# Kernel tuning notes

Hardware: AMD Instinct MI355X
Metric: run time of the kernel (lower is better)

## Reference

```python
import jax, jax.numpy as jnp
import numpy as np

NUM_TOKENS = 2048
HIDDEN = 2048
MOE_INTER = 1408
N_EXPERTS = 16
TOP_K = 4
N_SHARED = 2
SHARED_INTER = N_SHARED * MOE_INTER  # 2816
CAPACITY = 768
ROUTED_SCALE = 1.0


def setup_inputs() -> dict:
    key = jax.random.key(0)
    ks = jax.random.split(key, 9)
    s = 0.02  # init scale for stability
    return {
        "hidden_states": jax.random.normal(ks[0], (NUM_TOKENS, HIDDEN), jnp.float32),
        "w_gate": jax.random.normal(ks[1], (N_EXPERTS, HIDDEN), jnp.float32) * s,
        "w1": jax.random.normal(ks[2], (N_EXPERTS, HIDDEN, MOE_INTER), jnp.float32) * s,  # gate_proj
        "w3": jax.random.normal(ks[3], (N_EXPERTS, HIDDEN, MOE_INTER), jnp.float32) * s,  # up_proj
        "w2": jax.random.normal(ks[4], (N_EXPERTS, MOE_INTER, HIDDEN), jnp.float32) * s,  # down_proj
        "ws1": jax.random.normal(ks[5], (HIDDEN, SHARED_INTER), jnp.float32) * s,
        "ws3": jax.random.normal(ks[6], (HIDDEN, SHARED_INTER), jnp.float32) * s,
        "ws2": jax.random.normal(ks[7], (SHARED_INTER, HIDDEN), jnp.float32) * s,
    }


def _moe_forward(x, w_gate, w1, w3, w2, ws1, ws3, ws2):
    T, d = x.shape
    E = w1.shape[0]
    # ---- router: softmax scores, top-k selection (DeepSeek-V2, norm_topk_prob=False) ----
    scores = jax.nn.softmax(x @ w_gate.T, axis=-1)            # [T, E]
    topw, topi = jax.lax.top_k(scores, TOP_K)                 # [T, K]
    topw = topw * ROUTED_SCALE
    flat_e = topi.reshape(-1)                                 # [T*K] expert id per slot
    flat_w = topw.reshape(-1)                                 # [T*K]
    tok_ids = jnp.repeat(jnp.arange(T), TOP_K)                # [T*K]
    # ---- dispatch: position of each slot within its expert's buffer ----
    onehot = jax.nn.one_hot(flat_e, E, dtype=jnp.int32)       # [T*K, E]
    pos = jnp.take_along_axis(jnp.cumsum(onehot, axis=0), flat_e[:, None], axis=1)[:, 0] - 1
    valid = (pos < CAPACITY).astype(x.dtype)
    buf = jnp.zeros((E, CAPACITY, d), x.dtype).at[flat_e, pos].set(x[tok_ids], mode='drop')
    # ---- grouped SwiGLU expert FFN ----
    g = jnp.einsum('ecd,edi->eci', buf, w1)
    u = jnp.einsum('ecd,edi->eci', buf, w3)
    o = jnp.einsum('eci,eid->ecd', jax.nn.silu(g) * u, w2)    # [E, C, d]
    # ---- combine: gather back, weight, scatter-add per token ----
    gathered = o[flat_e, jnp.clip(pos, 0, CAPACITY - 1)] * (flat_w * valid)[:, None]
    routed = jax.ops.segment_sum(gathered, tok_ids, num_segments=T)  # [T, d]
    # ---- shared experts (always-on SwiGLU) ----
    shared = (jax.nn.silu(x @ ws1) * (x @ ws3)) @ ws2
    return routed + shared


def reference(hidden_states, w_gate, w1, w3, w2, ws1, ws3, ws2):
    return _moe_forward(hidden_states, w_gate, w1, w3, w2, ws1, ws3, ws2)
```

## Files before the change

kernel.cpp:

```cpp
#include <hip/hip_runtime.h>
#include <hip/hip_bf16.h>
#include <cstdint>

#define T_TOKENS 2048
#define HIDDEN 2048
#define INTER 1408
#define NEXP 16
#define TOPK 4
#define SINTER 2816
#define CAP 768
#define BK 32

typedef __attribute__((ext_vector_type(8))) short short8;
typedef __attribute__((ext_vector_type(8))) unsigned short ushort8;
typedef __attribute__((ext_vector_type(4))) float f32x4;

__device__ __forceinline__ float4 ld4f(const float* p) {
  return *reinterpret_cast<const float4*>(p);
}

__device__ __forceinline__ unsigned short f2bf(float v) {
  unsigned int u = __float_as_uint(v);
  unsigned int r = (u + 0x7FFFu + ((u >> 16) & 1u)) >> 16;
  return (unsigned short)r;
}

__device__ __forceinline__ void gld16(const void* g, void* l) {
  __builtin_amdgcn_global_load_lds(
      (const __attribute__((address_space(1))) void*)g,
      (__attribute__((address_space(3))) void*)l, 16, 0, 0);
}

__global__ __launch_bounds__(64) void router_kernel(
    const float* __restrict__ x, const float* __restrict__ wg,
    int* __restrict__ topi, float* __restrict__ topw)
{
  const int t = blockIdx.x;
  const int lane = threadIdx.x;
  float acc[NEXP];
#pragma unroll
  for (int e = 0; e < NEXP; ++e) acc[e] = 0.f;
  const float* xr = x + (size_t)t * HIDDEN;
  for (int i = lane; i < HIDDEN; i += 64) {
    float xv = xr[i];
#pragma unroll
    for (int e = 0; e < NEXP; ++e) acc[e] += xv * wg[e * HIDDEN + i];
  }
#pragma unroll
  for (int e = 0; e < NEXP; ++e) {
#pragma unroll
    for (int off = 32; off > 0; off >>= 1)
      acc[e] += __shfl_xor(acc[e], off);
  }
  float m = acc[0];
#pragma unroll
  for (int e = 1; e < NEXP; ++e) m = fmaxf(m, acc[e]);
  float p[NEXP];
  float s = 0.f;
#pragma unroll
  for (int e = 0; e < NEXP; ++e) { p[e] = expf(acc[e] - m); s += p[e]; }
  const float inv = 1.f / s;
#pragma unroll
  for (int e = 0; e < NEXP; ++e) p[e] *= inv;
  if (lane == 0) {
#pragma unroll
    for (int k = 0; k < TOPK; ++k) {
      float best = -1.f; int bi = 0;
#pragma unroll
      for (int e = 0; e < NEXP; ++e)
        if (p[e] > best) { best = p[e]; bi = e; }
      topi[t * TOPK + k] = bi;
      topw[t * TOPK + k] = best;
      p[bi] = -1.f;
    }
  }
}

__global__ __launch_bounds__(1024) void partition_kernel(
    const int* __restrict__ topi, float* __restrict__ topw,
    int* __restrict__ rowtok, int* __restrict__ count)
{
  __shared__ int se[T_TOKENS * TOPK];
  for (int i = threadIdx.x; i < T_TOKENS * TOPK; i += 1024) se[i] = topi[i];
  __syncthreads();

  const int wave = threadIdx.x >> 6;
  const int lane = threadIdx.x & 63;
  const uint64_t below = (lane == 0) ? 0ull : ((~0ull) >> (64 - lane));
  int base = 0;
  for (int c = 0; c < T_TOKENS * TOPK; c += 64) {
    int ev = se[c + lane];
    uint64_t mask = __ballot(ev == wave);
    if (ev == wave) {
      int my = base + __popcll(mask & below);
      if (my < CAP) rowtok[wave * CAP + my] = c + lane;
      else          topw[c + lane] = 0.f;
    }
    base += __popcll(mask);
  }
  if (lane == 0) count[wave] = base < CAP ? base : CAP;
}

__global__ __launch_bounds__(256) void cvt_x_kernel(
    const float* __restrict__ x, unsigned short* __restrict__ xb)
{
  const long i = ((long)blockIdx.x * 256 + threadIdx.x) * 8;
  float4 a = ld4f(x + i), b = ld4f(x + i + 4);
  float v[8] = {a.x, a.y, a.z, a.w, b.x, b.y, b.z, b.w};
  unsigned short o[8];
#pragma unroll
  for (int j = 0; j < 8; ++j) o[j] = f2bf(v[j]);
  *(ushort8*)(xb + i) = *(ushort8*)&o[0];
}

__global__ __launch_bounds__(256) void tcvt_w_kernel(
    const float* __restrict__ W, unsigned short* __restrict__ T,
    int K, int N, long tz, int mul, int which)
{
  const long z = blockIdx.z;
  W += z * (long)K * N;
  T += z * tz;
  const int k0 = blockIdx.x * 64, n0 = blockIdx.y * 64;
  __shared__ float tile[64][65];
  const int tr = threadIdx.x >> 4;
  const int tc4 = (threadIdx.x & 15) * 4;
#pragma unroll
  for (int p = 0; p < 4; ++p) {
    int r = p * 16 + tr;
    float4 v = ld4f(W + (long)(k0 + r) * N + n0 + tc4);
    tile[r][tc4] = v.x; tile[r][tc4 + 1] = v.y;
    tile[r][tc4 + 2] = v.z; tile[r][tc4 + 3] = v.w;
  }
  __syncthreads();
  const int wn = threadIdx.x >> 3;
  const int wk = (threadIdx.x & 7) * 8;
#pragma unroll
  for (int p = 0; p < 2; ++p) {
    int n = p * 32 + wn;
    unsigned short o[8];
#pragma unroll
    for (int j = 0; j < 8; ++j) o[j] = f2bf(tile[wk + j][n]);
    const int gn = n0 + n;
    const long prow = ((long)(gn >> 4) * mul + which) * 16 + (gn & 15);
    *(ushort8*)(T + prow * K + k0 + wk) = *(ushort8*)&o[0];
  }
}

template<int EPI>
__global__ __launch_bounds__(256, 2)
void gemm_bf(const unsigned short* __restrict__ Ag, int ldka,
             const unsigned short* __restrict__ Bg, long bstride,
             float* __restrict__ C, unsigned short* __restrict__ H, int ldc,
             const int* __restrict__ arows_g, int ashift, long aexp,
             const int* __restrict__ crows_g, long cexp,
             const int* __restrict__ cnt, int Mfix, int K,
             int MT, int NTn)
{
  const int nwg = gridDim.x;
  const int lin = (blockIdx.x & 7) * (nwg >> 3) + (blockIdx.x >> 3);
  const int mt = lin % MT;
  const int rest = lin / MT;
  const int nt = rest % NTn;
  const int e = rest / NTn;

  const int M = cnt ? cnt[e] : Mfix;
  if (mt * 128 >= M) return;
  const int n0 = nt * 128;

  const int tid = threadIdx.x;
  const int l = tid & 63;
  const int w = tid >> 6;
  const int wm = w >> 1;
  const int wn = w & 1;
  const int fr = l & 15;
  const int fc = l >> 4;

  const int* arows = arows_g ? arows_g + e * CAP : nullptr;
  const int* crows = crows_g ? crows_g + e * CAP : nullptr;
  const unsigned short* Bexp = Bg + (long)e * bstride;

  __shared__ __align__(16) unsigned short sA[3][128 * BK];
  __shared__ __align__(16) unsigned short sB[3][128 * BK];

  const int rb_s = ((l >> 3) & 1) | (((l >> 5) & 1) << 1);
  const int sch = ((l & 3) ^ rb_s) * 8;
  long aoff[2], boff[2];
#pragma unroll
  for (int j = 0; j < 2; ++j) {
    const int rloc = j * 64 + w * 16 + (l >> 2);
    int r = mt * 128 + rloc;
    if (r > M - 1) r = M - 1;
    const long arow = arows ? (long)(arows[r] >> ashift) : (aexp * e + r);
    aoff[j] = arow * (long)ldka + sch;
    boff[j] = (long)(n0 + rloc) * K + sch;
  }

  const int rb_r = ((fr >> 1) & 1) | (((fr >> 3) & 1) << 1);
  const int pcoff = (fc ^ rb_r) * 8;

  f32x4 acc[4][4];
#pragma unroll
  for (int i = 0; i < 4; ++i)
#pragma unroll
    for (int j = 0; j < 4; ++j) acc[i][j] = (f32x4)0.f;

  const int NT = K / BK;

  auto stage = [&](int buf, int kt) {
#pragma unroll
    for (int j = 0; j < 2; ++j) {
      gld16(Ag + aoff[j] + kt, &sA[buf][(j * 64 + w * 16) * BK]);
      gld16(Bexp + boff[j] + kt, &sB[buf][(j * 64 + w * 16) * BK]);
    }
  };

  stage(0, 0);
  stage(1, BK);

  int rb = 0, wb = 2;
  for (int t = 0; t < NT; ++t) {
    if (t + 1 < NT) asm volatile("s_waitcnt vmcnt(4)" ::: "memory");
    else            asm volatile("s_waitcnt vmcnt(0)" ::: "memory");
    __builtin_amdgcn_s_barrier();
    __builtin_amdgcn_sched_barrier(0);

    if (t + 2 < NT) stage(wb, (t + 2) * BK);

    short8 fa[4], fb[4];
#pragma unroll
    for (int mi = 0; mi < 4; ++mi)
      fa[mi] = *(const short8*)&sA[rb][(wm * 64 + mi * 16 + fr) * BK + pcoff];
#pragma unroll
    for (int ni = 0; ni < 4; ++ni)
      fb[ni] = *(const short8*)&sB[rb][(wn * 64 + ni * 16 + fr) * BK + pcoff];
#pragma unroll
    for (int mi = 0; mi < 4; ++mi)
#pragma unroll
      for (int ni = 0; ni < 4; ++ni)
        acc[mi][ni] = __builtin_amdgcn_mfma_f32_16x16x32_bf16(fa[mi], fb[ni], acc[mi][ni], 0, 0, 0);

    rb = (rb == 2) ? 0 : rb + 1;
    wb = (wb == 2) ? 0 : wb + 1;
  }

#pragma unroll
  for (int mi = 0; mi < 4; ++mi)
#pragma unroll
    for (int rr = 0; rr < 4; ++rr) {
      const int r = mt * 128 + wm * 64 + mi * 16 + fc * 4 + rr;
      if (r >= M) continue;
      const long crow = crows ? (long)crows[r] : (cexp * e + r);
      if constexpr (EPI == 2) {
#pragma unroll
        for (int np = 0; np < 2; ++np) {
          const float g = acc[mi][2 * np][rr];
          const float u = acc[mi][2 * np + 1][rr];
          const float h = u * (g / (1.f + __expf(-g)));
          const int i = (n0 / 32 + 2 * wn + np) * 16 + fr;
          H[crow * (long)ldc + i] = f2bf(h);
        }
      } else {
#pragma unroll
        for (int ni = 0; ni < 4; ++ni) {
          const int col = n0 + wn * 64 + ni * 16 + fr;
          C[crow * (long)ldc + col] = acc[mi][ni][rr];
        }
      }
    }
}

__global__ __launch_bounds__(256) void combine_kernel(
    const float* __restrict__ o_slot, const float* __restrict__ topw,
    float* __restrict__ out)
{
  const int t = blockIdx.x;
  float w[TOPK];
#pragma unroll
  for (int k = 0; k < TOPK; ++k) w[k] = topw[t * TOPK + k];
  float* orow = out + (size_t)t * HIDDEN;
  for (int c = threadIdx.x * 4; c < HIDDEN; c += 256 * 4) {
    float4 acc = *reinterpret_cast<float4*>(orow + c);
#pragma unroll
    for (int k = 0; k < TOPK; ++k) {
      if (w[k] != 0.f) {
        float4 v = ld4f(o_slot + ((size_t)(t * TOPK + k)) * HIDDEN + c);
        acc.x += w[k] * v.x; acc.y += w[k] * v.y;
        acc.z += w[k] * v.z; acc.w += w[k] * v.w;
      }
    }
    *reinterpret_cast<float4*>(orow + c) = acc;
  }
}

extern "C" void kernel_launch(void* const* d_in, const int* in_sizes, int n_in,
                              void* d_out, int out_size, void* d_ws, size_t ws_size,
                              hipStream_t stream)
{
  const float* x   = (const float*)d_in[0];
  const float* wg  = (const float*)d_in[1];
  const float* w1  = (const float*)d_in[2];
  const float* w3  = (const float*)d_in[3];
  const float* w2  = (const float*)d_in[4];
  const float* ws1 = (const float*)d_in[5];
  const float* ws3 = (const float*)d_in[6];
  const float* ws2 = (const float*)d_in[7];
  float* out = (float*)d_out;

  char* w = (char*)d_ws;
  int*   topi   = (int*)w;   w += (size_t)T_TOKENS * TOPK * 4;
  float* topw   = (float*)w; w += (size_t)T_TOKENS * TOPK * 4;
  int*   rowtok = (int*)w;   w += (size_t)NEXP * CAP * 4;
  int*   count  = (int*)w;   w += 256;
  uintptr_t a = (uintptr_t)w; a = (a + 255) & ~(uintptr_t)255; w = (char*)a;

  const size_t XSZ  = (size_t)T_TOKENS * HIDDEN;
  const size_t WSI  = (size_t)2 * HIDDEN * SINTER;
  const size_t WRI  = (size_t)2 * NEXP * HIDDEN * INTER;
  const size_t HSSZ = (size_t)T_TOKENS * SINTER;
  const size_t HRSZ = (size_t)NEXP * CAP * INTER;

  unsigned short* xb  = (unsigned short*)w; w += XSZ * 2;
  unsigned short* wSi = (unsigned short*)w; w += WSI * 2;
  unsigned short* wRi = (unsigned short*)w; w += WRI * 2;
  unsigned short* hs  = (unsigned short*)w; w += HSSZ * 2;
  unsigned short* hr  = (unsigned short*)w; w += HRSZ * 2;
  unsigned short* wS2 = wSi;
  unsigned short* wR2 = wRi;
  float* o_slot = (float*)(wRi + (size_t)NEXP * HIDDEN * INTER);

  router_kernel<<<T_TOKENS, 64, 0, stream>>>(x, wg, topi, topw);
  partition_kernel<<<1, 1024, 0, stream>>>(topi, topw, rowtok, count);
  cvt_x_kernel<<<(int)(XSZ / (256 * 8)), 256, 0, stream>>>(x, xb);

  tcvt_w_kernel<<<dim3(HIDDEN / 64, SINTER / 64, 1), 256, 0, stream>>>(
      ws1, wSi, HIDDEN, SINTER, 0L, 2, 0);
  tcvt_w_kernel<<<dim3(HIDDEN / 64, SINTER / 64, 1), 256, 0, stream>>>(
      ws3, wSi, HIDDEN, SINTER, 0L, 2, 1);
  gemm_bf<2><<<(T_TOKENS / 128) * (2 * SINTER / 128), 256, 0, stream>>>(
      xb, HIDDEN, wSi, 0L, nullptr, hs, SINTER,
      nullptr, 0, 0L, nullptr, 0L,
      nullptr, T_TOKENS, HIDDEN, T_TOKENS / 128, 2 * SINTER / 128);

  tcvt_w_kernel<<<dim3(HIDDEN / 64, INTER / 64, NEXP), 256, 0, stream>>>(
      w1, wRi, HIDDEN, INTER, (long)2 * HIDDEN * INTER, 2, 0);
  tcvt_w_kernel<<<dim3(HIDDEN / 64, INTER / 64, NEXP), 256, 0, stream>>>(
      w3, wRi, HIDDEN, INTER, (long)2 * HIDDEN * INTER, 2, 1);
  gemm_bf<2><<<(CAP / 128) * (2 * INTER / 128) * NEXP, 256, 0, stream>>>(
      xb, HIDDEN, wRi, (long)2 * HIDDEN * INTER, nullptr, hr, INTER,
      rowtok, 2, 0L, nullptr, (long)CAP,
      count, 0, HIDDEN, CAP / 128, 2 * INTER / 128);

  tcvt_w_kernel<<<dim3(SINTER / 64, HIDDEN / 64, 1), 256, 0, stream>>>(
      ws2, wS2, SINTER, HIDDEN, 0L, 1, 0);
  gemm_bf<0><<<(T_TOKENS / 128) * (HIDDEN / 128), 256, 0, stream>>>(
      hs, SINTER, wS2, 0L, out, nullptr, HIDDEN,
      nullptr, 0, 0L, nullptr, 0L,
      nullptr, T_TOKENS, SINTER, T_TOKENS / 128, HIDDEN / 128);

  tcvt_w_kernel<<<dim3(INTER / 64, HIDDEN / 64, NEXP), 256, 0, stream>>>(
      w2, wR2, INTER, HIDDEN, (long)INTER * HIDDEN, 1, 0);
  gemm_bf<0><<<(CAP / 128) * (HIDDEN / 128) * NEXP, 256, 0, stream>>>(
      hr, INTER, wR2, (long)INTER * HIDDEN, o_slot, nullptr, HIDDEN,
      nullptr, 0, (long)CAP, rowtok, 0L,
      count, 0, INTER, CAP / 128, HIDDEN / 128);

  combine_kernel<<<T_TOKENS, 256, 0, stream>>>(o_slot, topw, out);
}
```

Before: 635.8 us.

## Add 256x256-tile 8-wave GEMM with double-buffered swizzled LDS for three GEMMs

Introduces a new 512-thread GEMM kernel using 256x256 output tiles, BK=64 with double-buffered XOR-swizzled LDS, staged asynchronous global loads interleaved across eight sub-phases, and s_setprio around MFMA bursts. It replaces the 128x128 kernel for the shared gate/up GEMM and both routed-expert GEMMs, which should raise arithmetic intensity and overlap loads with compute. The shared down-projection still uses the old kernel, so its SwiGLU epilogue branch is dropped. Larger tiles cut the number of workgroups and waste more work on partially filled expert capacity tiles (per-expert counts are near 512 against a 768 capacity). They also need 128 KB of LDS per block, which may limit occupancy.

```diff
diff --git a/kernel.cpp b/kernel.cpp
--- a/kernel.cpp
+++ b/kernel.cpp
@@ -147,6 +147,178 @@
 }
 
 template<int EPI>
+__global__ __launch_bounds__(512, 2)
+void gemm_bf8(const unsigned short* __restrict__ Ag, int ldka,
+              const unsigned short* __restrict__ Bg, long bstride,
+              float* __restrict__ C, unsigned short* __restrict__ H, int ldc,
+              const int* __restrict__ arows_g, int ashift, long aexp,
+              const int* __restrict__ crows_g, long cexp,
+              const int* __restrict__ cnt, int Mfix, int K,
+              int MT, int NTn)
+{
+  const int nwg = gridDim.x;
+  const int lin = (blockIdx.x & 7) * (nwg >> 3) + (blockIdx.x >> 3);
+  const int mt = lin % MT;
+  const int rest = lin / MT;
+  const int nt = rest % NTn;
+  const int e = rest / NTn;
+
+  const int M = cnt ? cnt[e] : Mfix;
+  if (mt * 256 >= M) return;
+  const int n0 = nt * 256;
+
+  const int tid = threadIdx.x;
+  const int l = tid & 63;
+  const int w = tid >> 6;
+  const int wm = w >> 2;
+  const int wn = w & 3;
+  const int fr = l & 15;
+  const int fc = l >> 4;
+
+  const int* arows = arows_g ? arows_g + e * CAP : nullptr;
+  const int* crows = crows_g ? crows_g + e * CAP : nullptr;
+  const unsigned short* Bexp = Bg + (long)e * bstride;
+
+  __shared__ __align__(16) unsigned short sA[2][256 * 64];
+  __shared__ __align__(16) unsigned short sB[2][256 * 64];
+
+  const int sc = ((l & 7) ^ ((l >> 3) & 7)) * 8;
+
+  long aoffq[2][2];
+#pragma unroll
+  for (int q = 0; q < 2; ++q)
+#pragma unroll
+    for (int j = 0; j < 2; ++j) {
+      const int rloc = j * 128 + q * 64 + w * 8 + (l >> 3);
+      int r = mt * 256 + rloc;
+      if (r > M - 1) r = M - 1;
+      const long arow = arows ? (long)(arows[r] >> ashift) : (aexp * e + r);
+      aoffq[q][j] = arow * (long)ldka + sc;
+    }
+  long boffq[2][2];
+#pragma unroll
+  for (int q = 0; q < 2; ++q)
+#pragma unroll
+    for (int j = 0; j < 2; ++j) {
+      const int rloc = j * 128 + (w >> 2) * 64 + q * 32 + (w & 3) * 8 + (l >> 3);
+      boffq[q][j] = (long)(n0 + rloc) * K + sc;
+    }
+
+  f32x4 acc[8][4];
+#pragma unroll
+  for (int i = 0; i < 8; ++i)
+#pragma unroll
+    for (int j = 0; j < 4; ++j) acc[i][j] = (f32x4)0.f;
+
+  const int NT2 = K / 64;
+  const int NITER = NT2 / 2;
+
+  auto stgAq = [&](int d, int q, int tile) {
+#pragma unroll
+    for (int j = 0; j < 2; ++j)
+      gld16(Ag + aoffq[q][j] + (long)tile * 64,
+            &sA[d][(j * 128 + q * 64 + w * 8) * 64]);
+  };
+  auto stgBq = [&](int d, int q, int tile) {
+#pragma unroll
+    for (int j = 0; j < 2; ++j)
+      gld16(Bexp + boffq[q][j] + (long)tile * 64,
+            &sB[d][(j * 128 + (w >> 2) * 64 + q * 32 + (w & 3) * 8) * 64]);
+  };
+
+  stgAq(0, 0, 0); stgBq(0, 0, 0); stgAq(0, 1, 0); stgBq(0, 1, 0);
+  stgAq(1, 0, 1); stgBq(1, 0, 1);
+  asm volatile("s_waitcnt vmcnt(4)" ::: "memory");
+  __builtin_amdgcn_s_barrier();
+
+  for (int it = 0; it < NITER; ++it) {
+    const int t0 = 2 * it;
+    const bool notlast = (it + 1 < NITER);
+#pragma unroll
+    for (int p = 0; p < 8; ++p) {
+      const int d = p >> 2;
+      const int mh = (p >> 1) & 1;
+      const int nh = p & 1;
+
+      if      (p == 0) stgAq(1, 1, t0 + 1);
+      else if (p == 1) stgBq(1, 1, t0 + 1);
+      else if (notlast) {
+        if      (p == 2) stgAq(0, 0, t0 + 2);
+        else if (p == 3) stgBq(0, 0, t0 + 2);
+        else if (p == 4) stgAq(0, 1, t0 + 2);
+        else if (p == 5) stgBq(0, 1, t0 + 2);
+        else if (p == 6) stgAq(1, 0, t0 + 3);
+        else             stgBq(1, 0, t0 + 3);
+      }
+
+      short8 fa[4][2], fb[2][2];
+#pragma unroll
+      for (int mi = 0; mi < 4; ++mi)
+#pragma unroll
+        for (int kk = 0; kk < 2; ++kk) {
+          const int row = wm * 128 + mh * 64 + mi * 16 + fr;
+          const int pc = (kk * 4 + fc) ^ (fr & 7);
+          fa[mi][kk] = *(const short8*)&sA[d][row * 64 + pc * 8];
+        }
+#pragma unroll
+      for (int ni = 0; ni < 2; ++ni)
+#pragma unroll
+        for (int kk = 0; kk < 2; ++kk) {
+          const int row = wn * 64 + nh * 32 + ni * 16 + fr;
+          const int pc = (kk * 4 + fc) ^ (fr & 7);
+          fb[ni][kk] = *(const short8*)&sB[d][row * 64 + pc * 8];
+        }
+
+      __builtin_amdgcn_s_barrier();
+      asm volatile("s_waitcnt lgkmcnt(0)" ::: "memory");
+      __builtin_amdgcn_sched_barrier(0);
+      __builtin_amdgcn_s_setprio(1);
+#pragma unroll
+      for (int mi = 0; mi < 4; ++mi)
+#pragma unroll
+        for (int ni = 0; ni < 2; ++ni)
+#pragma unroll
+          for (int kk = 0; kk < 2; ++kk)
+            acc[mh * 4 + mi][nh * 2 + ni] = __builtin_amdgcn_mfma_f32_16x16x32_bf16(
+                fa[mi][kk], fb[ni][kk], acc[mh * 4 + mi][nh * 2 + ni], 0, 0, 0);
+      __builtin_amdgcn_s_setprio(0);
+      if (p == 3) {
+        if (notlast) asm volatile("s_waitcnt vmcnt(4)" ::: "memory");
+        else         asm volatile("s_waitcnt vmcnt(0)" ::: "memory");
+      } else if (p == 7 && notlast) {
+        asm volatile("s_waitcnt vmcnt(4)" ::: "memory");
+      }
+      __builtin_amdgcn_s_barrier();
+    }
+  }
+
+#pragma unroll
+  for (int mi = 0; mi < 8; ++mi)
+#pragma unroll
+    for (int rr = 0; rr < 4; ++rr) {
+      const int r = mt * 256 + wm * 128 + mi * 16 + fc * 4 + rr;
+      if (r >= M) continue;
+      const long crow = crows ? (long)crows[r] : (cexp * e + r);
+      if constexpr (EPI == 2) {
+#pragma unroll
+        for (int nh = 0; nh < 2; ++nh) {
+          const float g = acc[mi][nh * 2 + 0][rr];
+          const float u = acc[mi][nh * 2 + 1][rr];
+          const float h = u * (g / (1.f + __expf(-g)));
+          const int i = (n0 / 32 + wn * 2 + nh) * 16 + fr;
+          H[crow * (long)ldc + i] = f2bf(h);
+        }
+      } else {
+#pragma unroll
+        for (int nj = 0; nj < 4; ++nj) {
+          const int col = n0 + wn * 64 + nj * 16 + fr;
+          C[crow * (long)ldc + col] = acc[mi][nj][rr];
+        }
+      }
+    }
+}
+
+template<int EPI>
 __global__ __launch_bounds__(256, 2)
 void gemm_bf(const unsigned short* __restrict__ Ag, int ldka,
              const unsigned short* __restrict__ Bg, long bstride,
@@ -250,21 +422,10 @@
       const int r = mt * 128 + wm * 64 + mi * 16 + fc * 4 + rr;
       if (r >= M) continue;
       const long crow = crows ? (long)crows[r] : (cexp * e + r);
-      if constexpr (EPI == 2) {
-#pragma unroll
-        for (int np = 0; np < 2; ++np) {
-          const float g = acc[mi][2 * np][rr];
-          const float u = acc[mi][2 * np + 1][rr];
-          const float h = u * (g / (1.f + __expf(-g)));
-          const int i = (n0 / 32 + 2 * wn + np) * 16 + fr;
-          H[crow * (long)ldc + i] = f2bf(h);
-        }
-      } else {
-#pragma unroll
-        for (int ni = 0; ni < 4; ++ni) {
-          const int col = n0 + wn * 64 + ni * 16 + fr;
-          C[crow * (long)ldc + col] = acc[mi][ni][rr];
-        }
+#pragma unroll
+      for (int ni = 0; ni < 4; ++ni) {
+        const int col = n0 + wn * 64 + ni * 16 + fr;
+        C[crow * (long)ldc + col] = acc[mi][ni][rr];
       }
     }
 }
@@ -336,19 +497,19 @@
       ws1, wSi, HIDDEN, SINTER, 0L, 2, 0);
   tcvt_w_kernel<<<dim3(HIDDEN / 64, SINTER / 64, 1), 256, 0, stream>>>(
       ws3, wSi, HIDDEN, SINTER, 0L, 2, 1);
-  gemm_bf<2><<<(T_TOKENS / 128) * (2 * SINTER / 128), 256, 0, stream>>>(
+  gemm_bf8<2><<<(T_TOKENS / 256) * (2 * SINTER / 256), 512, 0, stream>>>(
       xb, HIDDEN, wSi, 0L, nullptr, hs, SINTER,
       nullptr, 0, 0L, nullptr, 0L,
-      nullptr, T_TOKENS, HIDDEN, T_TOKENS / 128, 2 * SINTER / 128);
+      nullptr, T_TOKENS, HIDDEN, T_TOKENS / 256, 2 * SINTER / 256);
 
   tcvt_w_kernel<<<dim3(HIDDEN / 64, INTER / 64, NEXP), 256, 0, stream>>>(
       w1, wRi, HIDDEN, INTER, (long)2 * HIDDEN * INTER, 2, 0);
   tcvt_w_kernel<<<dim3(HIDDEN / 64, INTER / 64, NEXP), 256, 0, stream>>>(
       w3, wRi, HIDDEN, INTER, (long)2 * HIDDEN * INTER, 2, 1);
-  gemm_bf<2><<<(CAP / 128) * (2 * INTER / 128) * NEXP, 256, 0, stream>>>(
+  gemm_bf8<2><<<(CAP / 256) * (2 * INTER / 256) * NEXP, 512, 0, stream>>>(
       xb, HIDDEN, wRi, (long)2 * HIDDEN * INTER, nullptr, hr, INTER,
       rowtok, 2, 0L, nullptr, (long)CAP,
-      count, 0, HIDDEN, CAP / 128, 2 * INTER / 128);
+      count, 0, HIDDEN, CAP / 256, 2 * INTER / 256);
 
   tcvt_w_kernel<<<dim3(SINTER / 64, HIDDEN / 64, 1), 256, 0, stream>>>(
       ws2, wS2, SINTER, HIDDEN, 0L, 1, 0);
@@ -359,10 +520,10 @@
 
   tcvt_w_kernel<<<dim3(INTER / 64, HIDDEN / 64, NEXP), 256, 0, stream>>>(
       w2, wR2, INTER, HIDDEN, (long)INTER * HIDDEN, 1, 0);
-  gemm_bf<0><<<(CAP / 128) * (HIDDEN / 128) * NEXP, 256, 0, stream>>>(
+  gemm_bf8<0><<<(CAP / 256) * (HIDDEN / 256) * NEXP, 512, 0, stream>>>(
       hr, INTER, wR2, (long)INTER * HIDDEN, o_slot, nullptr, HIDDEN,
       nullptr, 0, (long)CAP, rowtok, 0L,
-      count, 0, INTER, CAP / 128, HIDDEN / 128);
+      count, 0, INTER, CAP / 256, HIDDEN / 256);
 
   combine_kernel<<<T_TOKENS, 256, 0, stream>>>(o_slot, topw, out);
 }
```

After: 774.0 us. 21.7% more time.
